# Performance work log

Hardware: AMD Instinct MI355X
Metric: run time of the kernel (lower is better)

Reference implementation:

```python
import jax, jax.numpy as jnp
import numpy as np

N_HID = 18  # hardcoded hidden width in the original module


def setup_inputs() -> dict:
    key = jax.random.key(0)
    ks = jax.random.split(key, 9)
    B, NODES, F = 262144, 5, 6
    scale = 0.1
    return {
        "x": jax.random.normal(ks[0], (B, NODES, F), dtype=jnp.float32),
        "Wf": jax.random.normal(ks[1], (F, N_HID), dtype=jnp.float32) * scale,
        "bf": jnp.zeros((N_HID,), dtype=jnp.float32),
        "Wm": jax.random.normal(ks[2], (2 * N_HID, N_HID), dtype=jnp.float32) * scale,
        "bm": jnp.zeros((N_HID,), dtype=jnp.float32),
        "Wu": jax.random.normal(ks[3], (3 * N_HID, N_HID), dtype=jnp.float32) * scale,
        "bu": jnp.zeros((N_HID,), dtype=jnp.float32),
        "Wr": jax.random.normal(ks[4], (5 * N_HID, 1), dtype=jnp.float32) * scale,
        "br": jnp.zeros((1,), dtype=jnp.float32),
    }


def reference(x, Wf, bf, Wm, bm, Wu, bu, Wr, br):
    # Node feature embedding: [B,5,F] -> [B,5,18]
    h = jnp.tanh(jnp.einsum("bnf,fh->bnh", x, Wf) + bf)
    U = h  # Ua..Ue initialized to a..e
    # Ring edges (a,b),(b,c),(c,d),(d,e),(e,a): pair each node with next node
    m_in = jnp.concatenate([U, jnp.roll(U, -1, axis=1)], axis=2)  # [B,5,36]
    M = jnp.tanh(jnp.einsum("bne,eh->bnh", m_in, Wm) + bm)  # edge i = (node i, node i+1)
    # Node i is updated with message from edge (i-1, i) -> roll messages by +1
    u_in = jnp.concatenate([jnp.roll(M, 1, axis=1), U, h], axis=2)  # [B,5,54]
    U = jnp.tanh(jnp.einsum("bne,eh->bnh", u_in, Wu) + bu)
    # Readout: concat Ua..Ue -> [B,90] -> [B,1]
    flat = U.reshape(U.shape[0], 5 * N_HID)
    return flat @ Wr + br
```

## Files before the change

kernel.cpp:

```cpp
#include <hip/hip_runtime.h>
#include <stdint.h>


#define NH 18
#define PSTR 132
#define NPL 99
#define WS_DW 4480
#define WS_BYTES (WS_DW * 4)

typedef _Float16 half8 __attribute__((ext_vector_type(8)));
typedef float float4v __attribute__((ext_vector_type(4)));
union AB { uint32_t u[4]; half8 v; };

__device__ __forceinline__ float fast_tanh(float x) {
    float t = __builtin_amdgcn_exp2f(x * 2.8853900817779268f);
    float r = __builtin_amdgcn_rcpf(t + 1.0f);
    return __builtin_fmaf(-2.0f, r, 1.0f);
}
__device__ __forceinline__ uint32_t pkh(float a, float b) {
    union { _Float16 h[2]; uint32_t u; } z;
    z.h[0] = (_Float16)a; z.h[1] = (_Float16)b; return z.u;
}

__global__ __launch_bounds__(640) void prep_kernel(
    const float* __restrict__ Wf, const float* __restrict__ bf,
    const float* __restrict__ Wm, const float* __restrict__ bm,
    const float* __restrict__ Wu, const float* __restrict__ bu,
    const float* __restrict__ Wr, void* __restrict__ ws)
{
    uint32_t* wsd = (uint32_t*)ws;
    float* wsf = (float*)ws;
    const int tid = threadIdx.x;
    const int f = tid >> 6, lane = tid & 63;
    const int q = lane >> 4, l15 = lane & 15;
    {
        int rt, ks, which;
        if (f < 2)      { which = 0; rt = f;            ks = 0; }
        else if (f < 6) { which = 1; rt = (f - 2) >> 1; ks = (f - 2) & 1; }
        else            { which = 2; rt = (f - 6) >> 1; ks = (f - 6) & 1; }
        const int m = rt * 16 + l15;
        for (int jp = 0; jp < 4; ++jp) {
            float v[2];
            for (int h = 0; h < 2; ++h) {
                int k = ks * 32 + q * 8 + jp * 2 + h;
                float val = 0.0f;
                if (m < NH) {
                    if (which == 0) {
                        if (k < 6) val = Wf[k * NH + m];
                        else if (k == 6) val = bf[m];
                    } else if (which == 1) {
                        if (k < 36) val = Wm[k * NH + m];
                        else if (k == 36) val = bm[m];
                    } else {
                        if (k < NH) val = Wu[k * NH + m];
                        else if (k < 36) val = Wu[k * NH + m] + Wu[(k + NH) * NH + m];
                        else if (k == 36) val = bu[m];
                    }
                }
                v[h] = val;
            }
            wsd[f * 256 + lane * 4 + jp] = pkh(v[0], v[1]);
        }
    }
    for (int i = tid; i < 1280; i += 640) {
        int nr = i >> 6, ln = i & 63;
        int n = nr >> 2, r = nr & 3;
        wsf[2560 + i] = Wr[n * NH + (ln >> 4) * 4 + r];
    }
    for (int i = tid; i < 640; i += 640) {
        int nr = i >> 6, ln = i & 63;
        int n = nr >> 1, r = nr & 1;
        wsf[3840 + i] = ((ln >> 4) == 0) ? Wr[n * NH + 16 + r] : 0.0f;
    }
}

#define MFMA16(A, Bv, Cv) __builtin_amdgcn_mfma_f32_16x16x32_f16((A).v, (Bv).v, (Cv), 0, 0, 0)

__global__ __launch_bounds__(256, 3) void mp_mfma(
    const float* __restrict__ x, const float* __restrict__ br,
    const uint32_t* __restrict__ ws, float* __restrict__ out, int B)
{
    __shared__ uint32_t lds[NPL * PSTR];
    const int tid = threadIdx.x;
    const int lane = tid & 63, w = tid >> 6;
    const int l15 = lane & 15, q = lane >> 4;
    const float* wsf = (const float*)ws;

    AB F[10];
    #pragma unroll
    for (int f = 0; f < 10; ++f) {
        const uint32_t* p = ws + f * 256 + lane * 4;
        F[f].u[0] = p[0]; F[f].u[1] = p[1]; F[f].u[2] = p[2]; F[f].u[3] = p[3];
    }
    float wrA[5][4], wrB[5][2];
    #pragma unroll
    for (int n = 0; n < 5; ++n) {
        #pragma unroll
        for (int r = 0; r < 4; ++r) wrA[n][r] = wsf[2560 + (n * 4 + r) * 64 + lane];
        #pragma unroll
        for (int r = 0; r < 2; ++r) wrB[n][r] = wsf[3840 + (n * 2 + r) * 64 + lane];
    }
    const float brv = br[0];
    const uint32_t ONE = 0x00003C00u;
    const float4v Z = {0.f, 0.f, 0.f, 0.f};

    float racc[2];
    #pragma unroll
    for (int t = 0; t < 2; ++t) {
        const int c = (w + 4 * t) * 16 + l15;
        const long long eg = (long long)blockIdx.x * 128 + c;

        uint32_t xpk[5][4];
        if (eg < (long long)B) {
            const float2* xp = (const float2*)x + eg * 15;
            #pragma unroll
            for (int n = 0; n < 5; ++n) {
                float2 a = xp[n * 3], b2 = xp[n * 3 + 1], d = xp[n * 3 + 2];
                xpk[n][0] = pkh(a.x, a.y); xpk[n][1] = pkh(b2.x, b2.y);
                xpk[n][2] = pkh(d.x, d.y); xpk[n][3] = ONE;
            }
        } else {
            #pragma unroll
            for (int n = 0; n < 5; ++n) {
                xpk[n][0] = 0; xpk[n][1] = 0; xpk[n][2] = 0; xpk[n][3] = ONE;
            }
        }
        const int qc = q * 4 * PSTR + c;
        const int qw = q * 2 * PSTR + c;

        #pragma unroll
        for (int n = 0; n < 5; ++n) {
            AB bx; bx.u[0] = xpk[n][0]; bx.u[1] = xpk[n][1];
                   bx.u[2] = xpk[n][2]; bx.u[3] = xpk[n][3];
            float4v C0 = MFMA16(F[0], bx, Z);
            float4v C1 = MFMA16(F[1], bx, Z);
            uint32_t p0 = pkh(fast_tanh(C0[0]), fast_tanh(C0[1]));
            uint32_t p1 = pkh(fast_tanh(C0[2]), fast_tanh(C0[3]));
            uint32_t p2 = pkh(fast_tanh(C1[0]), fast_tanh(C1[1]));
            const int P1 = n * 18;
            const int P2 = (n == 0) ? 81 : (n - 1) * 18 + 9;
            lds[P1 * PSTR + qw] = p0; lds[(P1 + 1) * PSTR + qw] = p1;
            lds[P2 * PSTR + qw] = p0; lds[(P2 + 1) * PSTR + qw] = p1;
            if (q == 0) { lds[(P1 + 8) * PSTR + c] = p2; lds[(P2 + 8) * PSTR + c] = p2; }
            if (n == 0) {
                lds[90 * PSTR + qw] = p0; lds[91 * PSTR + qw] = p1;
                if (q == 0) lds[98 * PSTR + c] = p2;
            }
        }

        #pragma unroll
        for (int n = 0; n < 5; ++n) {
            const int vb = n * 18;
            AB b0, b1;
            b0.u[0] = lds[vb * PSTR + qc];       b0.u[1] = lds[(vb + 1) * PSTR + qc];
            b0.u[2] = lds[(vb + 2) * PSTR + qc]; b0.u[3] = lds[(vb + 3) * PSTR + qc];
            b1.u[0] = lds[(vb + 16) * PSTR + c]; b1.u[1] = lds[(vb + 17) * PSTR + c];
            b1.u[2] = ONE; b1.u[3] = 0;
            float4v C0 = MFMA16(F[2], b0, Z); C0 = MFMA16(F[3], b1, C0);
            float4v C1 = MFMA16(F[4], b0, Z); C1 = MFMA16(F[5], b1, C1);
            uint32_t p0 = pkh(fast_tanh(C0[0]), fast_tanh(C0[1]));
            uint32_t p1 = pkh(fast_tanh(C0[2]), fast_tanh(C0[3]));
            uint32_t p2 = pkh(fast_tanh(C1[0]), fast_tanh(C1[1]));
            const int PM = n * 18 + 9;
            lds[PM * PSTR + qw] = p0; lds[(PM + 1) * PSTR + qw] = p1;
            if (q == 0) lds[(PM + 8) * PSTR + c] = p2;
        }

        float rc = 0.0f;
        #pragma unroll
        for (int n = 0; n < 5; ++n) {
            const int vb = (n == 0) ? 81 : (n - 1) * 18 + 9;
            AB b0, b1;
            b0.u[0] = lds[vb * PSTR + qc];       b0.u[1] = lds[(vb + 1) * PSTR + qc];
            b0.u[2] = lds[(vb + 2) * PSTR + qc]; b0.u[3] = lds[(vb + 3) * PSTR + qc];
            b1.u[0] = lds[(vb + 16) * PSTR + c]; b1.u[1] = lds[(vb + 17) * PSTR + c];
            b1.u[2] = ONE; b1.u[3] = 0;
            float4v C0 = MFMA16(F[6], b0, Z); C0 = MFMA16(F[7], b1, C0);
            float4v C1 = MFMA16(F[8], b0, Z); C1 = MFMA16(F[9], b1, C1);
            rc = __builtin_fmaf(fast_tanh(C0[0]), wrA[n][0], rc);
            rc = __builtin_fmaf(fast_tanh(C0[1]), wrA[n][1], rc);
            rc = __builtin_fmaf(fast_tanh(C0[2]), wrA[n][2], rc);
            rc = __builtin_fmaf(fast_tanh(C0[3]), wrA[n][3], rc);
            rc = __builtin_fmaf(fast_tanh(C1[0]), wrB[n][0], rc);
            rc = __builtin_fmaf(fast_tanh(C1[1]), wrB[n][1], rc);
        }
        racc[t] = rc;
    }

    #pragma unroll
    for (int t = 0; t < 2; ++t) {
        float s = racc[t];
        s += __shfl_xor(s, 16, 64);
        s += __shfl_xor(s, 32, 64);
        const int c = (w + 4 * t) * 16 + l15;
        const long long eg = (long long)blockIdx.x * 128 + c;
        if (q == 0 && eg < (long long)B) out[eg] = s + brv;
    }
}

__global__ __launch_bounds__(256) void mp_fallback(
    const float* __restrict__ x,
    const float* __restrict__ Wf, const float* __restrict__ bf,
    const float* __restrict__ Wm, const float* __restrict__ bm,
    const float* __restrict__ Wu, const float* __restrict__ bu,
    const float* __restrict__ Wr, const float* __restrict__ br,
    float* __restrict__ out, int B)
{
    __shared__ float sWf[6 * NH]; __shared__ float sbf[NH];
    __shared__ float sWm[36 * NH]; __shared__ float sbm[NH];
    __shared__ float sWuM[NH * NH]; __shared__ float sWuH[NH * NH];
    __shared__ float sbu[NH]; __shared__ float sWr[5 * NH];
    __shared__ float sx[256 * 30];
    const int tid = threadIdx.x;
    for (int i = tid; i < 6 * NH; i += 256) sWf[i] = Wf[i];
    for (int i = tid; i < 36 * NH; i += 256) sWm[i] = Wm[i];
    for (int i = tid; i < NH * NH; i += 256) {
        sWuM[i] = Wu[i];
        sWuH[i] = Wu[NH * NH + i] + Wu[2 * NH * NH + i];
    }
    for (int i = tid; i < 5 * NH; i += 256) sWr[i] = Wr[i];
    if (tid < NH) { sbf[tid] = bf[tid]; sbm[tid] = bm[tid]; sbu[tid] = bu[tid]; }
    const long long base = (long long)blockIdx.x * (256 * 30);
    const long long xtot = (long long)B * 30;
    for (int i = tid; i < 256 * 30; i += 256) {
        long long g = base + i;
        sx[i] = (g < xtot) ? x[g] : 0.0f;
    }
    __syncthreads();
    float h[5][NH];
    #pragma unroll
    for (int n = 0; n < 5; ++n) {
        float acc[NH];
        #pragma unroll
        for (int k = 0; k < NH; ++k) acc[k] = sbf[k];
        #pragma unroll
        for (int f = 0; f < 6; ++f) {
            float xf = sx[tid * 30 + n * 6 + f];
            #pragma unroll
            for (int k = 0; k < NH; ++k)
                acc[k] = __builtin_fmaf(xf, sWf[f * NH + k], acc[k]);
        }
        #pragma unroll
        for (int k = 0; k < NH; ++k) h[n][k] = fast_tanh(acc[k]);
    }
    float Mprev[NH];
    {
        float acc[NH];
        #pragma unroll
        for (int k = 0; k < NH; ++k) acc[k] = sbm[k];
        #pragma unroll
        for (int j = 0; j < NH; ++j) {
            float a = h[4][j], b = h[0][j];
            #pragma unroll
            for (int k = 0; k < NH; ++k)
                acc[k] = __builtin_fmaf(b, sWm[(NH + j) * NH + k],
                          __builtin_fmaf(a, sWm[j * NH + k], acc[k]));
        }
        #pragma unroll
        for (int k = 0; k < NH; ++k) Mprev[k] = fast_tanh(acc[k]);
    }
    float racc = br[0];
    #pragma unroll
    for (int n = 0; n < 5; ++n) {
        {
            float acc[NH];
            #pragma unroll
            for (int k = 0; k < NH; ++k) acc[k] = sbu[k];
            #pragma unroll
            for (int j = 0; j < NH; ++j) {
                float mval = Mprev[j], hv = h[n][j];
                #pragma unroll
                for (int k = 0; k < NH; ++k)
                    acc[k] = __builtin_fmaf(hv, sWuH[j * NH + k],
                              __builtin_fmaf(mval, sWuM[j * NH + k], acc[k]));
            }
            #pragma unroll
            for (int k = 0; k < NH; ++k)
                racc = __builtin_fmaf(fast_tanh(acc[k]), sWr[n * NH + k], racc);
        }
        if (n < 4) {
            float acc[NH];
            #pragma unroll
            for (int k = 0; k < NH; ++k) acc[k] = sbm[k];
            #pragma unroll
            for (int j = 0; j < NH; ++j) {
                float a = h[n][j], b = h[n + 1][j];
                #pragma unroll
                for (int k = 0; k < NH; ++k)
                    acc[k] = __builtin_fmaf(b, sWm[(NH + j) * NH + k],
                              __builtin_fmaf(a, sWm[j * NH + k], acc[k]));
            }
            #pragma unroll
            for (int k = 0; k < NH; ++k) Mprev[k] = fast_tanh(acc[k]);
        }
    }
    long long b = (long long)blockIdx.x * 256 + tid;
    if (b < B) out[b] = racc;
}

extern "C" void kernel_launch(void* const* d_in, const int* in_sizes, int n_in,
                              void* d_out, int out_size, void* d_ws, size_t ws_size,
                              hipStream_t stream) {
    const float* x  = (const float*)d_in[0];
    const float* Wf = (const float*)d_in[1];
    const float* bf = (const float*)d_in[2];
    const float* Wm = (const float*)d_in[3];
    const float* bm = (const float*)d_in[4];
    const float* Wu = (const float*)d_in[5];
    const float* bu = (const float*)d_in[6];
    const float* Wr = (const float*)d_in[7];
    const float* br = (const float*)d_in[8];
    float* out = (float*)d_out;
    const int B = in_sizes[0] / 30;

    if (ws_size >= WS_BYTES) {
        prep_kernel<<<1, 640, 0, stream>>>(Wf, bf, Wm, bm, Wu, bu, Wr, d_ws);
        const int grid = (B + 127) / 128;
        mp_mfma<<<grid, 256, 0, stream>>>(x, br, (const uint32_t*)d_ws, out, B);
    } else {
        const int grid = (B + 255) / 256;
        mp_fallback<<<grid, 256, 0, stream>>>(x, Wf, bf, Wm, bm, Wu, bu, Wr, br, out, B);
    }
}
```

Measured before the change: 121.2 us.

## Fuse weight prep into main kernel and halve per-block tile

Removes the separate single-block prep kernel and has every block pack the fp16 MFMA weight fragments into shared memory itself, then load them into registers. Each block now handles 64 samples instead of 128, with a smaller LDS stride and a launch bound of 6 blocks per SM, to raise occupancy. Only the q==0 lanes load x, which cuts redundant global reads. The cost is that every block repeats the weight packing from global memory, adds two barriers, and there are twice as many blocks.

```diff
diff --git a/kernel.cpp b/kernel.cpp
--- a/kernel.cpp
+++ b/kernel.cpp
@@ -3,10 +3,8 @@
 
 
 #define NH 18
-#define PSTR 132
+#define PSTR 68
 #define NPL 99
-#define WS_DW 4480
-#define WS_BYTES (WS_DW * 4)
 
 typedef _Float16 half8 __attribute__((ext_vector_type(8)));
 typedef float float4v __attribute__((ext_vector_type(4)));
@@ -22,27 +20,33 @@
     z.h[0] = (_Float16)a; z.h[1] = (_Float16)b; return z.u;
 }
 
-__global__ __launch_bounds__(640) void prep_kernel(
+#define MFMA16(A, Bv, Cv) __builtin_amdgcn_mfma_f32_16x16x32_f16((A).v, (Bv).v, (Cv), 0, 0, 0)
+
+__global__ __launch_bounds__(256, 6) void mp_mfma(
+    const float* __restrict__ x,
     const float* __restrict__ Wf, const float* __restrict__ bf,
     const float* __restrict__ Wm, const float* __restrict__ bm,
     const float* __restrict__ Wu, const float* __restrict__ bu,
-    const float* __restrict__ Wr, void* __restrict__ ws)
+    const float* __restrict__ Wr, const float* __restrict__ br,
+    float* __restrict__ out, int B)
 {
-    uint32_t* wsd = (uint32_t*)ws;
-    float* wsf = (float*)ws;
+    __shared__ uint32_t lds[NPL * PSTR];
     const int tid = threadIdx.x;
-    const int f = tid >> 6, lane = tid & 63;
-    const int q = lane >> 4, l15 = lane & 15;
-    {
+    const int lane = tid & 63, w = tid >> 6;
+    const int l15 = lane & 15, q = lane >> 4;
+
+    for (int v = tid; v < 640; v += 256) {
+        const int fi = v >> 6, ln = v & 63;
+        const int fq = ln >> 4, fl = ln & 15;
         int rt, ks, which;
-        if (f < 2)      { which = 0; rt = f;            ks = 0; }
-        else if (f < 6) { which = 1; rt = (f - 2) >> 1; ks = (f - 2) & 1; }
-        else            { which = 2; rt = (f - 6) >> 1; ks = (f - 6) & 1; }
-        const int m = rt * 16 + l15;
+        if (fi < 2)      { which = 0; rt = fi;           ks = 0; }
+        else if (fi < 6) { which = 1; rt = (fi - 2) >> 1; ks = (fi - 2) & 1; }
+        else             { which = 2; rt = (fi - 6) >> 1; ks = (fi - 6) & 1; }
+        const int m = rt * 16 + fl;
         for (int jp = 0; jp < 4; ++jp) {
-            float v[2];
-            for (int h = 0; h < 2; ++h) {
-                int k = ks * 32 + q * 8 + jp * 2 + h;
+            float vv[2];
+            for (int hh = 0; hh < 2; ++hh) {
+                int k = ks * 32 + fq * 8 + jp * 2 + hh;
                 float val = 0.0f;
                 if (m < NH) {
                     if (which == 0) {
@@ -57,245 +61,115 @@
                         else if (k == 36) val = bu[m];
                     }
                 }
-                v[h] = val;
+                vv[hh] = val;
             }
-            wsd[f * 256 + lane * 4 + jp] = pkh(v[0], v[1]);
+            lds[fi * 256 + ln * 4 + jp] = pkh(vv[0], vv[1]);
         }
     }
-    for (int i = tid; i < 1280; i += 640) {
-        int nr = i >> 6, ln = i & 63;
-        int n = nr >> 2, r = nr & 3;
-        wsf[2560 + i] = Wr[n * NH + (ln >> 4) * 4 + r];
-    }
-    for (int i = tid; i < 640; i += 640) {
-        int nr = i >> 6, ln = i & 63;
-        int n = nr >> 1, r = nr & 1;
-        wsf[3840 + i] = ((ln >> 4) == 0) ? Wr[n * NH + 16 + r] : 0.0f;
-    }
-}
-
-#define MFMA16(A, Bv, Cv) __builtin_amdgcn_mfma_f32_16x16x32_f16((A).v, (Bv).v, (Cv), 0, 0, 0)
-
-__global__ __launch_bounds__(256, 3) void mp_mfma(
-    const float* __restrict__ x, const float* __restrict__ br,
-    const uint32_t* __restrict__ ws, float* __restrict__ out, int B)
-{
-    __shared__ uint32_t lds[NPL * PSTR];
-    const int tid = threadIdx.x;
-    const int lane = tid & 63, w = tid >> 6;
-    const int l15 = lane & 15, q = lane >> 4;
-    const float* wsf = (const float*)ws;
-
+    __syncthreads();
     AB F[10];
     #pragma unroll
     for (int f = 0; f < 10; ++f) {
-        const uint32_t* p = ws + f * 256 + lane * 4;
-        F[f].u[0] = p[0]; F[f].u[1] = p[1]; F[f].u[2] = p[2]; F[f].u[3] = p[3];
+        const int o = f * 256 + lane * 4;
+        F[f].u[0] = lds[o];     F[f].u[1] = lds[o + 1];
+        F[f].u[2] = lds[o + 2]; F[f].u[3] = lds[o + 3];
     }
+    __syncthreads();
+
     float wrA[5][4], wrB[5][2];
     #pragma unroll
     for (int n = 0; n < 5; ++n) {
         #pragma unroll
-        for (int r = 0; r < 4; ++r) wrA[n][r] = wsf[2560 + (n * 4 + r) * 64 + lane];
+        for (int r = 0; r < 4; ++r) wrA[n][r] = Wr[n * NH + q * 4 + r];
         #pragma unroll
-        for (int r = 0; r < 2; ++r) wrB[n][r] = wsf[3840 + (n * 2 + r) * 64 + lane];
+        for (int r = 0; r < 2; ++r) wrB[n][r] = (q == 0) ? Wr[n * NH + 16 + r] : 0.0f;
     }
     const float brv = br[0];
     const uint32_t ONE = 0x00003C00u;
     const float4v Z = {0.f, 0.f, 0.f, 0.f};
 
-    float racc[2];
+    const int c = w * 16 + l15;
+    const long long eg = (long long)blockIdx.x * 64 + c;
+
+    uint32_t xpk[5][4];
     #pragma unroll
-    for (int t = 0; t < 2; ++t) {
-        const int c = (w + 4 * t) * 16 + l15;
-        const long long eg = (long long)blockIdx.x * 128 + c;
-
-        uint32_t xpk[5][4];
-        if (eg < (long long)B) {
-            const float2* xp = (const float2*)x + eg * 15;
-            #pragma unroll
-            for (int n = 0; n < 5; ++n) {
-                float2 a = xp[n * 3], b2 = xp[n * 3 + 1], d = xp[n * 3 + 2];
-                xpk[n][0] = pkh(a.x, a.y); xpk[n][1] = pkh(b2.x, b2.y);
-                xpk[n][2] = pkh(d.x, d.y); xpk[n][3] = ONE;
-            }
-        } else {
-            #pragma unroll
-            for (int n = 0; n < 5; ++n) {
-                xpk[n][0] = 0; xpk[n][1] = 0; xpk[n][2] = 0; xpk[n][3] = ONE;
-            }
-        }
-        const int qc = q * 4 * PSTR + c;
-        const int qw = q * 2 * PSTR + c;
-
+    for (int n = 0; n < 5; ++n) {
+        xpk[n][0] = 0; xpk[n][1] = 0; xpk[n][2] = 0;
+        xpk[n][3] = (q == 0) ? ONE : 0;
+    }
+    if (q == 0 && eg < (long long)B) {
+        const float2* xp = (const float2*)x + eg * 15;
         #pragma unroll
         for (int n = 0; n < 5; ++n) {
-            AB bx; bx.u[0] = xpk[n][0]; bx.u[1] = xpk[n][1];
-                   bx.u[2] = xpk[n][2]; bx.u[3] = xpk[n][3];
-            float4v C0 = MFMA16(F[0], bx, Z);
-            float4v C1 = MFMA16(F[1], bx, Z);
-            uint32_t p0 = pkh(fast_tanh(C0[0]), fast_tanh(C0[1]));
-            uint32_t p1 = pkh(fast_tanh(C0[2]), fast_tanh(C0[3]));
-            uint32_t p2 = pkh(fast_tanh(C1[0]), fast_tanh(C1[1]));
-            const int P1 = n * 18;
-            const int P2 = (n == 0) ? 81 : (n - 1) * 18 + 9;
-            lds[P1 * PSTR + qw] = p0; lds[(P1 + 1) * PSTR + qw] = p1;
-            lds[P2 * PSTR + qw] = p0; lds[(P2 + 1) * PSTR + qw] = p1;
-            if (q == 0) { lds[(P1 + 8) * PSTR + c] = p2; lds[(P2 + 8) * PSTR + c] = p2; }
-            if (n == 0) {
-                lds[90 * PSTR + qw] = p0; lds[91 * PSTR + qw] = p1;
-                if (q == 0) lds[98 * PSTR + c] = p2;
-            }
+            float2 a = xp[n * 3], b2 = xp[n * 3 + 1], d = xp[n * 3 + 2];
+            xpk[n][0] = pkh(a.x, a.y); xpk[n][1] = pkh(b2.x, b2.y);
+            xpk[n][2] = pkh(d.x, d.y);
         }
+    }
+    const int qc = q * 4 * PSTR + c;
+    const int qw = q * 2 * PSTR + c;
 
-        #pragma unroll
-        for (int n = 0; n < 5; ++n) {
-            const int vb = n * 18;
-            AB b0, b1;
-            b0.u[0] = lds[vb * PSTR + qc];       b0.u[1] = lds[(vb + 1) * PSTR + qc];
-            b0.u[2] = lds[(vb + 2) * PSTR + qc]; b0.u[3] = lds[(vb + 3) * PSTR + qc];
-            b1.u[0] = lds[(vb + 16) * PSTR + c]; b1.u[1] = lds[(vb + 17) * PSTR + c];
-            b1.u[2] = ONE; b1.u[3] = 0;
-            float4v C0 = MFMA16(F[2], b0, Z); C0 = MFMA16(F[3], b1, C0);
-            float4v C1 = MFMA16(F[4], b0, Z); C1 = MFMA16(F[5], b1, C1);
-            uint32_t p0 = pkh(fast_tanh(C0[0]), fast_tanh(C0[1]));
-            uint32_t p1 = pkh(fast_tanh(C0[2]), fast_tanh(C0[3]));
-            uint32_t p2 = pkh(fast_tanh(C1[0]), fast_tanh(C1[1]));
-            const int PM = n * 18 + 9;
-            lds[PM * PSTR + qw] = p0; lds[(PM + 1) * PSTR + qw] = p1;
-            if (q == 0) lds[(PM + 8) * PSTR + c] = p2;
+    #pragma unroll
+    for (int n = 0; n < 5; ++n) {
+        AB bx; bx.u[0] = xpk[n][0]; bx.u[1] = xpk[n][1];
+               bx.u[2] = xpk[n][2]; bx.u[3] = xpk[n][3];
+        float4v C0 = MFMA16(F[0], bx, Z);
+        float4v C1 = MFMA16(F[1], bx, Z);
+        uint32_t p0 = pkh(fast_tanh(C0[0]), fast_tanh(C0[1]));
+        uint32_t p1 = pkh(fast_tanh(C0[2]), fast_tanh(C0[3]));
+        uint32_t p2 = pkh(fast_tanh(C1[0]), fast_tanh(C1[1]));
+        const int P1 = n * 18;
+        const int P2 = (n == 0) ? 81 : (n - 1) * 18 + 9;
+        lds[P1 * PSTR + qw] = p0; lds[(P1 + 1) * PSTR + qw] = p1;
+        lds[P2 * PSTR + qw] = p0; lds[(P2 + 1) * PSTR + qw] = p1;
+        if (q == 0) { lds[(P1 + 8) * PSTR + c] = p2; lds[(P2 + 8) * PSTR + c] = p2; }
+        if (n == 0) {
+            lds[90 * PSTR + qw] = p0; lds[91 * PSTR + qw] = p1;
+            if (q == 0) lds[98 * PSTR + c] = p2;
         }
-
-        float rc = 0.0f;
-        #pragma unroll
-        for (int n = 0; n < 5; ++n) {
-            const int vb = (n == 0) ? 81 : (n - 1) * 18 + 9;
-            AB b0, b1;
-            b0.u[0] = lds[vb * PSTR + qc];       b0.u[1] = lds[(vb + 1) * PSTR + qc];
-            b0.u[2] = lds[(vb + 2) * PSTR + qc]; b0.u[3] = lds[(vb + 3) * PSTR + qc];
-            b1.u[0] = lds[(vb + 16) * PSTR + c]; b1.u[1] = lds[(vb + 17) * PSTR + c];
-            b1.u[2] = ONE; b1.u[3] = 0;
-            float4v C0 = MFMA16(F[6], b0, Z); C0 = MFMA16(F[7], b1, C0);
-            float4v C1 = MFMA16(F[8], b0, Z); C1 = MFMA16(F[9], b1, C1);
-            rc = __builtin_fmaf(fast_tanh(C0[0]), wrA[n][0], rc);
-            rc = __builtin_fmaf(fast_tanh(C0[1]), wrA[n][1], rc);
-            rc = __builtin_fmaf(fast_tanh(C0[2]), wrA[n][2], rc);
-            rc = __builtin_fmaf(fast_tanh(C0[3]), wrA[n][3], rc);
-            rc = __builtin_fmaf(fast_tanh(C1[0]), wrB[n][0], rc);
-            rc = __builtin_fmaf(fast_tanh(C1[1]), wrB[n][1], rc);
-        }
-        racc[t] = rc;
     }
 
     #pragma unroll
-    for (int t = 0; t < 2; ++t) {
-        float s = racc[t];
-        s += __shfl_xor(s, 16, 64);
-        s += __shfl_xor(s, 32, 64);
-        const int c = (w + 4 * t) * 16 + l15;
-        const long long eg = (long long)blockIdx.x * 128 + c;
-        if (q == 0 && eg < (long long)B) out[eg] = s + brv;
+    for (int n = 0; n < 5; ++n) {
+        const int vb = n * 18;
+        AB b0, b1;
+        b0.u[0] = lds[vb * PSTR + qc];       b0.u[1] = lds[(vb + 1) * PSTR + qc];
+        b0.u[2] = lds[(vb + 2) * PSTR + qc]; b0.u[3] = lds[(vb + 3) * PSTR + qc];
+        b1.u[0] = lds[(vb + 16) * PSTR + c]; b1.u[1] = lds[(vb + 17) * PSTR + c];
+        b1.u[2] = ONE; b1.u[3] = 0;
+        float4v C0 = MFMA16(F[2], b0, Z); C0 = MFMA16(F[3], b1, C0);
+        float4v C1 = MFMA16(F[4], b0, Z); C1 = MFMA16(F[5], b1, C1);
+        uint32_t p0 = pkh(fast_tanh(C0[0]), fast_tanh(C0[1]));
+        uint32_t p1 = pkh(fast_tanh(C0[2]), fast_tanh(C0[3]));
+        uint32_t p2 = pkh(fast_tanh(C1[0]), fast_tanh(C1[1]));
+        const int PM = n * 18 + 9;
+        lds[PM * PSTR + qw] = p0; lds[(PM + 1) * PSTR + qw] = p1;
+        if (q == 0) lds[(PM + 8) * PSTR + c] = p2;
     }
-}
 
-__global__ __launch_bounds__(256) void mp_fallback(
-    const float* __restrict__ x,
-    const float* __restrict__ Wf, const float* __restrict__ bf,
-    const float* __restrict__ Wm, const float* __restrict__ bm,
-    const float* __restrict__ Wu, const float* __restrict__ bu,
-    const float* __restrict__ Wr, const float* __restrict__ br,
-    float* __restrict__ out, int B)
-{
-    __shared__ float sWf[6 * NH]; __shared__ float sbf[NH];
-    __shared__ float sWm[36 * NH]; __shared__ float sbm[NH];
-    __shared__ float sWuM[NH * NH]; __shared__ float sWuH[NH * NH];
-    __shared__ float sbu[NH]; __shared__ float sWr[5 * NH];
-    __shared__ float sx[256 * 30];
-    const int tid = threadIdx.x;
-    for (int i = tid; i < 6 * NH; i += 256) sWf[i] = Wf[i];
-    for (int i = tid; i < 36 * NH; i += 256) sWm[i] = Wm[i];
-    for (int i = tid; i < NH * NH; i += 256) {
-        sWuM[i] = Wu[i];
-        sWuH[i] = Wu[NH * NH + i] + Wu[2 * NH * NH + i];
-    }
-    for (int i = tid; i < 5 * NH; i += 256) sWr[i] = Wr[i];
-    if (tid < NH) { sbf[tid] = bf[tid]; sbm[tid] = bm[tid]; sbu[tid] = bu[tid]; }
-    const long long base = (long long)blockIdx.x * (256 * 30);
-    const long long xtot = (long long)B * 30;
-    for (int i = tid; i < 256 * 30; i += 256) {
-        long long g = base + i;
-        sx[i] = (g < xtot) ? x[g] : 0.0f;
-    }
-    __syncthreads();
-    float h[5][NH];
+    float rc = 0.0f;
     #pragma unroll
     for (int n = 0; n < 5; ++n) {
-        float acc[NH];
-        #pragma unroll
-        for (int k = 0; k < NH; ++k) acc[k] = sbf[k];
-        #pragma unroll
-        for (int f = 0; f < 6; ++f) {
-            float xf = sx[tid * 30 + n * 6 + f];
-            #pragma unroll
-            for (int k = 0; k < NH; ++k)
-                acc[k] = __builtin_fmaf(xf, sWf[f * NH + k], acc[k]);
-        }
-        #pragma unroll
-        for (int k = 0; k < NH; ++k) h[n][k] = fast_tanh(acc[k]);
+        const int vb = (n == 0) ? 81 : (n - 1) * 18 + 9;
+        AB b0, b1;
+        b0.u[0] = lds[vb * PSTR + qc];       b0.u[1] = lds[(vb + 1) * PSTR + qc];
+        b0.u[2] = lds[(vb + 2) * PSTR + qc]; b0.u[3] = lds[(vb + 3) * PSTR + qc];
+        b1.u[0] = lds[(vb + 16) * PSTR + c]; b1.u[1] = lds[(vb + 17) * PSTR + c];
+        b1.u[2] = ONE; b1.u[3] = 0;
+        float4v C0 = MFMA16(F[6], b0, Z); C0 = MFMA16(F[7], b1, C0);
+        float4v C1 = MFMA16(F[8], b0, Z); C1 = MFMA16(F[9], b1, C1);
+        rc = __builtin_fmaf(fast_tanh(C0[0]), wrA[n][0], rc);
+        rc = __builtin_fmaf(fast_tanh(C0[1]), wrA[n][1], rc);
+        rc = __builtin_fmaf(fast_tanh(C0[2]), wrA[n][2], rc);
+        rc = __builtin_fmaf(fast_tanh(C0[3]), wrA[n][3], rc);
+        rc = __builtin_fmaf(fast_tanh(C1[0]), wrB[n][0], rc);
+        rc = __builtin_fmaf(fast_tanh(C1[1]), wrB[n][1], rc);
     }
-    float Mprev[NH];
-    {
-        float acc[NH];
-        #pragma unroll
-        for (int k = 0; k < NH; ++k) acc[k] = sbm[k];
-        #pragma unroll
-        for (int j = 0; j < NH; ++j) {
-            float a = h[4][j], b = h[0][j];
-            #pragma unroll
-            for (int k = 0; k < NH; ++k)
-                acc[k] = __builtin_fmaf(b, sWm[(NH + j) * NH + k],
-                          __builtin_fmaf(a, sWm[j * NH + k], acc[k]));
-        }
-        #pragma unroll
-        for (int k = 0; k < NH; ++k) Mprev[k] = fast_tanh(acc[k]);
-    }
-    float racc = br[0];
-    #pragma unroll
-    for (int n = 0; n < 5; ++n) {
-        {
-            float acc[NH];
-            #pragma unroll
-            for (int k = 0; k < NH; ++k) acc[k] = sbu[k];
-            #pragma unroll
-            for (int j = 0; j < NH; ++j) {
-                float mval = Mprev[j], hv = h[n][j];
-                #pragma unroll
-                for (int k = 0; k < NH; ++k)
-                    acc[k] = __builtin_fmaf(hv, sWuH[j * NH + k],
-                              __builtin_fmaf(mval, sWuM[j * NH + k], acc[k]));
-            }
-            #pragma unroll
-            for (int k = 0; k < NH; ++k)
-                racc = __builtin_fmaf(fast_tanh(acc[k]), sWr[n * NH + k], racc);
-        }
-        if (n < 4) {
-            float acc[NH];
-            #pragma unroll
-            for (int k = 0; k < NH; ++k) acc[k] = sbm[k];
-            #pragma unroll
-            for (int j = 0; j < NH; ++j) {
-                float a = h[n][j], b = h[n + 1][j];
-                #pragma unroll
-                for (int k = 0; k < NH; ++k)
-                    acc[k] = __builtin_fmaf(b, sWm[(NH + j) * NH + k],
-                              __builtin_fmaf(a, sWm[j * NH + k], acc[k]));
-            }
-            #pragma unroll
-            for (int k = 0; k < NH; ++k) Mprev[k] = fast_tanh(acc[k]);
-        }
-    }
-    long long b = (long long)blockIdx.x * 256 + tid;
-    if (b < B) out[b] = racc;
+
+    float s = rc;
+    s += __shfl_xor(s, 16, 64);
+    s += __shfl_xor(s, 32, 64);
+    if (q == 0 && eg < (long long)B) out[eg] = s + brv;
 }
 
 extern "C" void kernel_launch(void* const* d_in, const int* in_sizes, int n_in,
@@ -312,13 +186,6 @@
     const float* br = (const float*)d_in[8];
     float* out = (float*)d_out;
     const int B = in_sizes[0] / 30;
-
-    if (ws_size >= WS_BYTES) {
-        prep_kernel<<<1, 640, 0, stream>>>(Wf, bf, Wm, bm, Wu, bu, Wr, d_ws);
-        const int grid = (B + 127) / 128;
-        mp_mfma<<<grid, 256, 0, stream>>>(x, br, (const uint32_t*)d_ws, out, B);
-    } else {
-        const int grid = (B + 255) / 256;
-        mp_fallback<<<grid, 256, 0, stream>>>(x, Wf, bf, Wm, bm, Wu, bu, Wr, br, out, B);
-    }
+    const int grid = (B + 63) / 64;
+    mp_mfma<<<grid, 256, 0, stream>>>(x, Wf, bf, Wm, bm, Wu, bu, Wr, br, out, B);
 }
```

Result: slower. 147.5 us (+21.7%).
